# Kernel optimization log

Hardware: AMD Instinct MI355X
Metric: run time of the kernel (lower is better)

Reference implementation:

```python
import jax, jax.numpy as jnp
import numpy as np

N_E = 1024
E_DIM = 512
BETA = 0.25


def setup_inputs() -> dict:
    key = jax.random.key(0)
    k1, k2 = jax.random.split(key)
    z = jax.random.normal(k1, (16, E_DIM, 64, 64), dtype=jnp.float32)
    # nn.Embedding default init: N(0,1)
    codebook = jax.random.normal(k2, (N_E, E_DIM), dtype=jnp.float32)
    return {"z": z, "codebook": codebook}


def reference(z, codebook):
    # z: [B, C, H, W] -> [B, H, W, C]
    zp = jnp.transpose(z, (0, 2, 3, 1))
    B, H, W, C = zp.shape
    zf = zp.reshape(-1, C)  # [N, e_dim]
    d = (jnp.sum(zf * zf, axis=1, keepdims=True)
         + jnp.sum(codebook * codebook, axis=1)
         - 2.0 * zf @ codebook.T)
    idx = jnp.argmin(d, axis=1)  # [N]
    # one-hot @ codebook == gather
    z_q = codebook[idx].reshape(B, H, W, C)
    sg = jax.lax.stop_gradient
    e_latent_loss = jnp.mean((sg(z_q) - zp) ** 2)
    q_latent_loss = jnp.mean((z_q - sg(zp)) ** 2)
    codebook_loss = q_latent_loss + BETA * e_latent_loss
    # straight-through estimator
    z_q_st = zp + sg(z_q - zp)
    z_q_out = jnp.transpose(z_q_st, (0, 3, 1, 2))  # [B, C, H, W]
    indices = idx.reshape(B, 1, H, W)
    return (z_q_out, codebook_loss, indices)
```

## Files before the change

kernel.cpp:

```cpp
#include <hip/hip_runtime.h>

#define N_E    1024
#define E_DIM  512
#define BATCH  16
#define HW     4096
#define NROW   (BATCH * HW)
#define ZQ_SIZE (BATCH * E_DIM * HW)
#define LOSS_OFF ZQ_SIZE
#define IDX_OFF (ZQ_SIZE + 1)

typedef _Float16 half_t;
typedef __attribute__((ext_vector_type(2)))  __fp16   fp16x2;
typedef __attribute__((ext_vector_type(8)))  _Float16 frag8;
typedef __attribute__((ext_vector_type(16))) float    accv;

union U32H2 { fp16x2 h; uint32_t u; };
union FragU { uint32_t u[4]; frag8 f; };

static __device__ inline uint32_t pack2(float a, float b) {
    U32H2 t; t.h = __builtin_amdgcn_cvt_pkrtz(a, b); return t.u;
}

__global__ void k_prep(const float* __restrict__ cb,
                       float* __restrict__ cn,
                       float* __restrict__ ct,
                       unsigned long long* __restrict__ best) {
    __shared__ float t[32][33];
    int tx = threadIdx.x & 31;
    int ty = threadIdx.x >> 5;
    int jt = blockIdx.x & 31;
    int ctl = blockIdx.x >> 5;
    int j0 = jt * 32, c0 = ctl * 32;
    #pragma unroll
    for (int i = 0; i < 4; i++) {
        int row = ty + i * 8;
        t[row][tx] = cb[(size_t)(j0 + row) * E_DIM + c0 + tx];
    }
    __syncthreads();
    #pragma unroll
    for (int i = 0; i < 4; i++) {
        int row = ty + i * 8;
        ct[(size_t)(c0 + row) * N_E + j0 + tx] = t[tx][row];
    }

    if (blockIdx.x < 256) {
        int lane = threadIdx.x & 63;
        int wid  = threadIdx.x >> 6;
        int j = blockIdx.x * 4 + wid;
        const float* row = cb + (size_t)j * E_DIM;
        float s = 0.f;
        #pragma unroll
        for (int k = 0; k < E_DIM; k += 64) {
            float v = row[k + lane];
            s += v * v;
        }
        #pragma unroll
        for (int m = 32; m >= 1; m >>= 1) s += __shfl_xor(s, m);
        if (lane == 0) cn[j] = s;
    }

    int g = blockIdx.x * 256 + threadIdx.x;
    if (g < NROW) best[g] = 0xFFFFFFFFFFFFFFFFull;
}

#define ASTR 44
#define BSTR 40

__global__ __launch_bounds__(256, 2) void k_argmin_mfma(
        const float* __restrict__ z,
        const float* __restrict__ cb,
        const float* __restrict__ cn,
        unsigned long long* __restrict__ best) {
    __shared__ uint32_t aP[128 * ASTR];
    __shared__ half_t   bH[128 * BSTR];
    __shared__ half_t   bL[128 * BSTR];

    int tid  = threadIdx.x;
    int lane = tid & 63;
    int l31  = lane & 31;
    int lh   = lane >> 5;
    int wm   = (tid >> 6) & 1;
    int wg   = tid >> 7;

    int jt    = blockIdx.x & 7;
    int mtile = blockIdx.x >> 3;
    int n0  = mtile * 128;
    int b   = n0 >> 12;
    int hw0 = n0 & 4095;
    const float* zA = z + (size_t)b * E_DIM * HW + hw0 + 4 * (tid & 31);
    int a_kq = tid >> 5;
    int b_kq = tid & 7;
    int b_j0 = tid >> 3;

    accv acc[2][2];
    #pragma unroll
    for (int mt = 0; mt < 2; mt++)
        #pragma unroll
        for (int nt = 0; nt < 2; nt++)
            #pragma unroll
            for (int i = 0; i < 16; i++) acc[mt][nt][i] = 0.f;

    for (int ks = 0; ks < 16; ks++) {
        int c0 = ks * 32;
        __syncthreads();
        {
            uint32_t pk[4][4];
            #pragma unroll
            for (int i = 0; i < 4; i++) {
                int k = a_kq * 4 + i;
                float4 v = *(const float4*)(zA + (size_t)(c0 + k) * HW);
                uint32_t H01 = pack2(v.x, v.y);
                uint32_t H23 = pack2(v.z, v.w);
                U32H2 h01; h01.u = H01; U32H2 h23; h23.u = H23;
                uint32_t L01 = pack2(v.x - (float)h01.h.x, v.y - (float)h01.h.y);
                uint32_t L23 = pack2(v.z - (float)h23.h.x, v.w - (float)h23.h.y);
                pk[0][i] = __builtin_amdgcn_perm(L01, H01, 0x05040100u);
                pk[1][i] = __builtin_amdgcn_perm(L01, H01, 0x07060302u);
                pk[2][i] = __builtin_amdgcn_perm(L23, H23, 0x05040100u);
                pk[3][i] = __builtin_amdgcn_perm(L23, H23, 0x07060302u);
            }
            int m0 = (tid & 31) * 4;
            #pragma unroll
            for (int r = 0; r < 4; r++) {
                int row = m0 + r;
                int qs = a_kq ^ ((row >> 3) & 7);
                uint4 w = make_uint4(pk[r][0], pk[r][1], pk[r][2], pk[r][3]);
                *(uint4*)&aP[row * ASTR + qs * 4] = w;
            }
        }
        {
            const float* cbB = cb + (size_t)(jt * 128) * E_DIM + c0 + b_kq * 4;
            #pragma unroll
            for (int r = 0; r < 4; r++) {
                int jl = b_j0 + 32 * r;
                float4 v = *(const float4*)(cbB + (size_t)jl * E_DIM);
                uint32_t H01 = pack2(v.x, v.y);
                uint32_t H23 = pack2(v.z, v.w);
                U32H2 h01; h01.u = H01; U32H2 h23; h23.u = H23;
                uint32_t L01 = pack2(v.x - (float)h01.h.x, v.y - (float)h01.h.y);
                uint32_t L23 = pack2(v.z - (float)h23.h.x, v.w - (float)h23.h.y);
                *(uint2*)&bH[jl * BSTR + b_kq * 4] = make_uint2(H01, H23);
                *(uint2*)&bL[jl * BSTR + b_kq * 4] = make_uint2(L01, L23);
            }
        }
        __syncthreads();

        #pragma unroll
        for (int ks2 = 0; ks2 < 2; ks2++) {
            int k0 = ks2 * 16 + lh * 8;
            int q0 = k0 >> 2;
            frag8 ah[2], al[2];
            #pragma unroll
            for (int mt = 0; mt < 2; mt++) {
                int row = wm * 64 + mt * 32 + l31;
                int sw  = (row >> 3) & 7;
                const uint32_t* pr = &aP[row * ASTR];
                uint4 q0v = *(const uint4*)(pr + ((q0 ^ sw) << 2));
                uint4 q1v = *(const uint4*)(pr + (((q0 + 1) ^ sw) << 2));
                FragU uh, ul;
                uh.u[0] = __builtin_amdgcn_perm(q0v.y, q0v.x, 0x05040100u);
                uh.u[1] = __builtin_amdgcn_perm(q0v.w, q0v.z, 0x05040100u);
                uh.u[2] = __builtin_amdgcn_perm(q1v.y, q1v.x, 0x05040100u);
                uh.u[3] = __builtin_amdgcn_perm(q1v.w, q1v.z, 0x05040100u);
                ul.u[0] = __builtin_amdgcn_perm(q0v.y, q0v.x, 0x07060302u);
                ul.u[1] = __builtin_amdgcn_perm(q0v.w, q0v.z, 0x07060302u);
                ul.u[2] = __builtin_amdgcn_perm(q1v.y, q1v.x, 0x07060302u);
                ul.u[3] = __builtin_amdgcn_perm(q1v.w, q1v.z, 0x07060302u);
                ah[mt] = uh.f; al[mt] = ul.f;
            }
            frag8 bh[2], bl[2];
            #pragma unroll
            for (int nt = 0; nt < 2; nt++) {
                int n = wg * 64 + nt * 32 + l31;
                bh[nt] = *(const frag8*)&bH[n * BSTR + k0];
                bl[nt] = *(const frag8*)&bL[n * BSTR + k0];
            }
            #pragma unroll
            for (int mt = 0; mt < 2; mt++)
                #pragma unroll
                for (int nt = 0; nt < 2; nt++) {
                    acc[mt][nt] = __builtin_amdgcn_mfma_f32_32x32x16_f16(
                        ah[mt], bh[nt], acc[mt][nt], 0, 0, 0);
                    acc[mt][nt] = __builtin_amdgcn_mfma_f32_32x32x16_f16(
                        ah[mt], bl[nt], acc[mt][nt], 0, 0, 0);
                    acc[mt][nt] = __builtin_amdgcn_mfma_f32_32x32x16_f16(
                        al[mt], bh[nt], acc[mt][nt], 0, 0, 0);
                }
        }
    }

    int jbase = jt * 128 + wg * 64;
    float cn0 = cn[jbase + l31];
    float cn1 = cn[jbase + 32 + l31];
    int j0i = jbase + l31, j1i = jbase + 32 + l31;
    #pragma unroll
    for (int mt = 0; mt < 2; mt++) {
        #pragma unroll
        for (int r = 0; r < 16; r++) {
            float d0 = cn0 - 2.f * acc[mt][0][r];
            float d1 = cn1 - 2.f * acc[mt][1][r];
            float v; int ix;
            if (d1 < d0) { v = d1; ix = j1i; } else { v = d0; ix = j0i; }
            #pragma unroll
            for (int m = 1; m <= 16; m <<= 1) {
                float ov = __shfl_xor(v, m);
                int   oi = __shfl_xor(ix, m);
                if (ov < v || (ov == v && oi < ix)) { v = ov; ix = oi; }
            }
            if (l31 == r) {
                int row = wm * 64 + mt * 32 + (r & 3) + 8 * (r >> 2) + 4 * lh;
                uint32_t s = __float_as_uint(v);
                uint32_t k32 = (s & 0x80000000u) ? ~s : (s | 0x80000000u);
                unsigned long long key =
                    ((unsigned long long)k32 << 32) | (uint32_t)ix;
                atomicMin(&best[n0 + row], key);
            }
        }
    }
}

__global__ void k_gather_loss(const float* __restrict__ z,
                              const float* __restrict__ ct,
                              const unsigned long long* __restrict__ best,
                              float* __restrict__ out,
                              float* __restrict__ pl) {
    int g = blockIdx.x * blockDim.x + threadIdx.x;
    int w4 = g & 1023;
    int bc = g >> 10;
    int c  = bc & 511;
    int b  = bc >> 9;
    int n4 = b * 1024 + w4;

    ulonglong2 b01 = *(const ulonglong2*)(best + (size_t)n4 * 4);
    ulonglong2 b23 = *(const ulonglong2*)(best + (size_t)n4 * 4 + 2);
    int4 iv;
    iv.x = (int)(uint32_t)b01.x; iv.y = (int)(uint32_t)b01.y;
    iv.z = (int)(uint32_t)b23.x; iv.w = (int)(uint32_t)b23.y;

    const float* ctc = ct + (size_t)c * N_E;
    float4 zq;
    zq.x = ctc[iv.x]; zq.y = ctc[iv.y]; zq.z = ctc[iv.z]; zq.w = ctc[iv.w];
    float4 zv = *(const float4*)(z + (size_t)g * 4);

    float4 d;
    d.x = zq.x - zv.x; d.y = zq.y - zv.y; d.z = zq.z - zv.z; d.w = zq.w - zv.w;
    float4 o;
    o.x = zv.x + d.x; o.y = zv.y + d.y; o.z = zv.z + d.z; o.w = zv.w + d.w;
    *(float4*)(out + (size_t)g * 4) = o;

    float ls = d.x * d.x + d.y * d.y + d.z * d.z + d.w * d.w;
    #pragma unroll
    for (int m = 32; m >= 1; m >>= 1) ls += __shfl_xor(ls, m);

    __shared__ float wsum[4];
    int lane = threadIdx.x & 63, wid = threadIdx.x >> 6;
    if (lane == 0) wsum[wid] = ls;
    __syncthreads();
    if (threadIdx.x == 0)
        pl[blockIdx.x] = wsum[0] + wsum[1] + wsum[2] + wsum[3];

    if (c == 0) {
        float* ip = out + IDX_OFF + (size_t)n4 * 4;
        ip[0] = (float)iv.x; ip[1] = (float)iv.y;
        ip[2] = (float)iv.z; ip[3] = (float)iv.w;
    }
}

__global__ void k_final(const float* __restrict__ pl, float* __restrict__ out) {
    float s = 0.f;
    for (int i = threadIdx.x; i < 8192; i += 256) s += pl[i];
    #pragma unroll
    for (int m = 32; m >= 1; m >>= 1) s += __shfl_xor(s, m);
    __shared__ float wsum[4];
    int lane = threadIdx.x & 63, wid = threadIdx.x >> 6;
    if (lane == 0) wsum[wid] = s;
    __syncthreads();
    if (threadIdx.x == 0) {
        float tot = wsum[0] + wsum[1] + wsum[2] + wsum[3];
        out[LOSS_OFF] = 1.25f * tot / (float)ZQ_SIZE;
    }
}

extern "C" void kernel_launch(void* const* d_in, const int* in_sizes, int n_in,
                              void* d_out, int out_size, void* d_ws, size_t ws_size,
                              hipStream_t stream) {
    const float* z  = (const float*)d_in[0];
    const float* cb = (const float*)d_in[1];
    float* out = (float*)d_out;

    float* cn = (float*)d_ws + 16;
    float* ct = cn + 1024;
    unsigned long long* best =
        (unsigned long long*)(ct + 512 * 1024);
    float* pl = (float*)(best + NROW);

    k_prep<<<512, 256, 0, stream>>>(cb, cn, ct, best);
    k_argmin_mfma<<<4096, 256, 0, stream>>>(z, cb, cn, best);
    k_gather_loss<<<ZQ_SIZE / 4 / 256, 256, 0, stream>>>(z, ct, best, out, pl);
    k_final<<<1, 256, 0, stream>>>(pl, out);
}
```

Measured before the change: 560.4 us.

## Prepack codebook fp16 tiles and loop all codes per block with DMA pipeline

Precomputes the split fp16 high/low codebook tiles in a swizzled layout (stored temporarily in the output buffer) and makes each argmin block loop over all 1024 codes for its 128 rows. This removes the redundant per-block codebook conversion, the 64-bit atomicMin traffic and the best-key initialisation. Codebook tiles are double-buffered through direct global-to-LDS loads, with the z tile loaded into registers one stage ahead. The running minimum is kept in registers and resolved across waves in LDS. The trade-off is more register pressure and a grid of only 512 blocks, which may limit occupancy and latency hiding.

```diff
diff --git a/kernel.cpp b/kernel.cpp
--- a/kernel.cpp
+++ b/kernel.cpp
@@ -1,4 +1,5 @@
 #include <hip/hip_runtime.h>
+#include <stdint.h>
 
 #define N_E    1024
 #define E_DIM  512
@@ -15,65 +16,85 @@
 typedef __attribute__((ext_vector_type(16))) float    accv;
 
 union U32H2 { fp16x2 h; uint32_t u; };
-union FragU { uint32_t u[4]; frag8 f; };
 
 static __device__ inline uint32_t pack2(float a, float b) {
     U32H2 t; t.h = __builtin_amdgcn_cvt_pkrtz(a, b); return t.u;
 }
 
-__global__ void k_prep(const float* __restrict__ cb,
+static __device__ __forceinline__ void dma16(const void* g, void* l) {
+    __builtin_amdgcn_global_load_lds(
+        (const __attribute__((address_space(1))) void*)g,
+        (__attribute__((address_space(3))) void*)l,
+        16, 0, 0);
+}
+
+__global__ void k_pack(const float* __restrict__ cb,
+                       uint32_t* __restrict__ cbP,
                        float* __restrict__ cn,
-                       float* __restrict__ ct,
-                       unsigned long long* __restrict__ best) {
-    __shared__ float t[32][33];
-    int tx = threadIdx.x & 31;
-    int ty = threadIdx.x >> 5;
-    int jt = blockIdx.x & 31;
-    int ctl = blockIdx.x >> 5;
-    int j0 = jt * 32, c0 = ctl * 32;
-    #pragma unroll
-    for (int i = 0; i < 4; i++) {
-        int row = ty + i * 8;
-        t[row][tx] = cb[(size_t)(j0 + row) * E_DIM + c0 + tx];
-    }
-    __syncthreads();
-    #pragma unroll
-    for (int i = 0; i < 4; i++) {
-        int row = ty + i * 8;
-        ct[(size_t)(c0 + row) * N_E + j0 + tx] = t[tx][row];
-    }
-
-    if (blockIdx.x < 256) {
-        int lane = threadIdx.x & 63;
-        int wid  = threadIdx.x >> 6;
-        int j = blockIdx.x * 4 + wid;
-        const float* row = cb + (size_t)j * E_DIM;
-        float s = 0.f;
-        #pragma unroll
-        for (int k = 0; k < E_DIM; k += 64) {
-            float v = row[k + lane];
-            s += v * v;
-        }
-        #pragma unroll
-        for (int m = 32; m >= 1; m >>= 1) s += __shfl_xor(s, m);
-        if (lane == 0) cn[j] = s;
-    }
-
-    int g = blockIdx.x * 256 + threadIdx.x;
-    if (g < NROW) best[g] = 0xFFFFFFFFFFFFFFFFull;
-}
-
-#define ASTR 44
-#define BSTR 40
+                       float* __restrict__ ct) {
+    __shared__ float tsh[32][33];
+    int bidx = blockIdx.x;
+    int tid  = threadIdx.x;
+
+    if (bidx < 128) {
+        int jt = bidx >> 4, ks = bidx & 15;
+        int kq = tid & 7, jb = tid >> 3;
+        uint32_t* tile = cbP + (size_t)bidx * 4096;
+        int sH = kq >> 1, o = (kq & 1) * 2;
+        #pragma unroll
+        for (int r = 0; r < 4; r++) {
+            int j = jb + 32 * r;
+            float4 v = *(const float4*)(cb + (size_t)(jt * 128 + j) * E_DIM + ks * 32 + kq * 4);
+            uint32_t H01 = pack2(v.x, v.y);
+            uint32_t H23 = pack2(v.z, v.w);
+            U32H2 h01; h01.u = H01; U32H2 h23; h23.u = H23;
+            uint32_t L01 = pack2(v.x - (float)h01.h.x, v.y - (float)h01.h.y);
+            uint32_t L23 = pack2(v.z - (float)h23.h.x, v.w - (float)h23.h.y);
+            int dH = ((sH)     ^ (j & 7)) * 4 + o;
+            int dL = ((sH + 4) ^ (j & 7)) * 4 + o;
+            *(uint2*)(tile + j * 32 + dH) = make_uint2(H01, H23);
+            *(uint2*)(tile + j * 32 + dL) = make_uint2(L01, L23);
+        }
+    } else {
+        int pb = bidx - 128;
+        int tx = tid & 31, ty = tid >> 5;
+        int jtp = pb & 31, ctl = pb >> 5;
+        int j0 = jtp * 32, c0 = ctl * 32;
+        #pragma unroll
+        for (int i = 0; i < 4; i++) {
+            int row = ty + i * 8;
+            tsh[row][tx] = cb[(size_t)(j0 + row) * E_DIM + c0 + tx];
+        }
+        __syncthreads();
+        #pragma unroll
+        for (int i = 0; i < 4; i++) {
+            int row = ty + i * 8;
+            ct[(size_t)(c0 + row) * N_E + j0 + tx] = tsh[tx][row];
+        }
+        if (pb < 256) {
+            int lane = tid & 63;
+            int wvid = tid >> 6;
+            int j = pb * 4 + wvid;
+            const float* rowp = cb + (size_t)j * E_DIM;
+            float s = 0.f;
+            #pragma unroll
+            for (int k = 0; k < E_DIM; k += 64) {
+                float v = rowp[k + lane];
+                s += v * v;
+            }
+            #pragma unroll
+            for (int m = 32; m >= 1; m >>= 1) s += __shfl_xor(s, m);
+            if (lane == 0) cn[j] = s;
+        }
+    }
+}
 
 __global__ __launch_bounds__(256, 2) void k_argmin_mfma(
         const float* __restrict__ z,
-        const float* __restrict__ cb,
+        const uint32_t* __restrict__ cbP,
         const float* __restrict__ cn,
-        unsigned long long* __restrict__ best) {
-    __shared__ uint32_t aP[128 * ASTR];
-    __shared__ half_t   bH[128 * BSTR];
-    __shared__ half_t   bL[128 * BSTR];
+        uint32_t* __restrict__ bestIdx) {
+    __shared__ uint32_t lds[16384];
 
     int tid  = threadIdx.x;
     int lane = tid & 63;
@@ -81,16 +102,27 @@
     int lh   = lane >> 5;
     int wm   = (tid >> 6) & 1;
     int wg   = tid >> 7;
-
-    int jt    = blockIdx.x & 7;
-    int mtile = blockIdx.x >> 3;
-    int n0  = mtile * 128;
-    int b   = n0 >> 12;
-    int hw0 = n0 & 4095;
-    const float* zA = z + (size_t)b * E_DIM * HW + hw0 + 4 * (tid & 31);
-    int a_kq = tid >> 5;
-    int b_kq = tid & 7;
-    int b_j0 = tid >> 3;
+    int wid  = tid >> 6;
+
+    int n0  = blockIdx.x * 128;
+    int b   = n0 >> 12, hw0 = n0 & 4095;
+
+    int arow  = tid & 127;
+    int khalf = tid >> 7;
+    const float* zBase = z + (size_t)b * E_DIM * HW + hw0 + arow;
+
+    const char* cT  = (const char*)cbP;
+    int uoff  = wid * 4096;
+    int goffB = uoff + lane * 16;
+
+    float cnv[16];
+    #pragma unroll
+    for (int j = 0; j < 8; j++) {
+        cnv[2 * j]     = cn[j * 128 + wg * 64 + l31];
+        cnv[2 * j + 1] = cn[j * 128 + wg * 64 + 32 + l31];
+    }
+    #pragma unroll
+    for (int q = 0; q < 16; q++) asm volatile("" :: "v"(cnv[q]));
 
     accv acc[2][2];
     #pragma unroll
@@ -100,107 +132,147 @@
             #pragma unroll
             for (int i = 0; i < 16; i++) acc[mt][nt][i] = 0.f;
 
-    for (int ks = 0; ks < 16; ks++) {
-        int c0 = ks * 32;
-        __syncthreads();
+    float bv[2][16];
+    int   bi[2][16];
+    #pragma unroll
+    for (int mt = 0; mt < 2; mt++)
+        #pragma unroll
+        for (int r = 0; r < 16; r++) { bv[mt][r] = 1e30f; bi[mt][r] = 0; }
+
+    float rA[16];
+
+    #define ALOAD(q) do {                                                      \
+        int c0_ = ((q) & 15) * 32 + khalf * 16;                                \
+        _Pragma("unroll")                                                      \
+        for (int i = 0; i < 16; i++)                                           \
+            rA[i] = zBase[(size_t)(c0_ + i) * HW];                             \
+    } while (0)
+
+    #define ACONV(q) do {                                                      \
+        uint32_t* at_ = lds + ((q) & 1) * 8192;                                \
+        int sw_ = arow & 7;                                                    \
+        uint32_t h_[8], l_[8];                                                 \
+        _Pragma("unroll")                                                      \
+        for (int i2 = 0; i2 < 8; i2++) {                                       \
+            uint32_t H = pack2(rA[2 * i2], rA[2 * i2 + 1]);                    \
+            U32H2 hh; hh.u = H;                                                \
+            uint32_t L = pack2(rA[2 * i2]     - (float)hh.h.x,                 \
+                               rA[2 * i2 + 1] - (float)hh.h.y);                \
+            h_[i2] = H; l_[i2] = L;                                            \
+        }                                                                      \
+        int s0_ = khalf * 2;                                                   \
+        *(uint4*)&at_[arow * 32 + (((s0_    ) ^ sw_) << 2)] =                  \
+            make_uint4(h_[0], h_[1], h_[2], h_[3]);                            \
+        *(uint4*)&at_[arow * 32 + (((s0_ + 1) ^ sw_) << 2)] =                  \
+            make_uint4(h_[4], h_[5], h_[6], h_[7]);                            \
+        *(uint4*)&at_[arow * 32 + (((s0_ + 4) ^ sw_) << 2)] =                  \
+            make_uint4(l_[0], l_[1], l_[2], l_[3]);                            \
+        *(uint4*)&at_[arow * 32 + (((s0_ + 5) ^ sw_) << 2)] =                  \
+            make_uint4(l_[4], l_[5], l_[6], l_[7]);                            \
+    } while (0)
+
+    #define BSTAGE(q) do {                                                     \
+        char* lb_ = (char*)lds + ((q) & 1) * 32768 + 16384 + uoff;             \
+        const char* gb_ = cT + (size_t)(q) * 16384 + goffB;                    \
+        dma16(gb_,        lb_);                                                \
+        dma16(gb_ + 1024, lb_ + 1024);                                         \
+        dma16(gb_ + 2048, lb_ + 2048);                                         \
+        dma16(gb_ + 3072, lb_ + 3072);                                         \
+    } while (0)
+
+    ALOAD(0);
+    BSTAGE(0);
+    asm volatile("s_waitcnt vmcnt(4)" ::: "memory");
+    ACONV(0);
+    ALOAD(1);
+    asm volatile("s_waitcnt lgkmcnt(0)" ::: "memory");
+    asm volatile("s_waitcnt vmcnt(16)" ::: "memory");
+    __builtin_amdgcn_s_barrier();
+
+    #pragma unroll
+    for (int jt = 0; jt < 8; jt++) {
+        #pragma unroll 1
+        for (int ks = 0; ks < 16; ks++) {
+            int p = jt * 16 + ks, pn = p + 1;
+            if (pn < 128) {
+                BSTAGE(pn);
+                asm volatile("s_waitcnt vmcnt(4)" ::: "memory");
+                ACONV(pn);
+                if (pn < 127) ALOAD(pn + 1);
+            }
+
+            const uint32_t* A = lds + (p & 1) * 8192;
+            const uint32_t* B = A + 4096;
+            __builtin_amdgcn_s_setprio(1);
+            #pragma unroll
+            for (int ks2 = 0; ks2 < 2; ks2++) {
+                int s = ks2 * 2 + lh;
+                frag8 ah[2], al[2], bh[2], bl[2];
+                #pragma unroll
+                for (int mt = 0; mt < 2; mt++) {
+                    int row = wm * 64 + mt * 32 + l31;
+                    int sw = row & 7;
+                    ah[mt] = *(const frag8*)&A[row * 32 + ((s ^ sw) << 2)];
+                    al[mt] = *(const frag8*)&A[row * 32 + (((s + 4) ^ sw) << 2)];
+                }
+                #pragma unroll
+                for (int nt = 0; nt < 2; nt++) {
+                    int n = wg * 64 + nt * 32 + l31;
+                    int sw = n & 7;
+                    bh[nt] = *(const frag8*)&B[n * 32 + ((s ^ sw) << 2)];
+                    bl[nt] = *(const frag8*)&B[n * 32 + (((s + 4) ^ sw) << 2)];
+                }
+                #pragma unroll
+                for (int mt = 0; mt < 2; mt++)
+                    #pragma unroll
+                    for (int nt = 0; nt < 2; nt++)
+                        acc[mt][nt] = __builtin_amdgcn_mfma_f32_32x32x16_f16(
+                            ah[mt], bh[nt], acc[mt][nt], 0, 0, 0);
+                #pragma unroll
+                for (int mt = 0; mt < 2; mt++)
+                    #pragma unroll
+                    for (int nt = 0; nt < 2; nt++)
+                        acc[mt][nt] = __builtin_amdgcn_mfma_f32_32x32x16_f16(
+                            ah[mt], bl[nt], acc[mt][nt], 0, 0, 0);
+                #pragma unroll
+                for (int mt = 0; mt < 2; mt++)
+                    #pragma unroll
+                    for (int nt = 0; nt < 2; nt++)
+                        acc[mt][nt] = __builtin_amdgcn_mfma_f32_32x32x16_f16(
+                            al[mt], bh[nt], acc[mt][nt], 0, 0, 0);
+            }
+            __builtin_amdgcn_s_setprio(0);
+            asm volatile("s_waitcnt lgkmcnt(0)" ::: "memory");
+            if (pn < 128) {
+                if (pn < 127) asm volatile("s_waitcnt vmcnt(16)" ::: "memory");
+                else          asm volatile("s_waitcnt vmcnt(0)"  ::: "memory");
+                __builtin_amdgcn_s_barrier();
+            }
+        }
         {
-            uint32_t pk[4][4];
-            #pragma unroll
-            for (int i = 0; i < 4; i++) {
-                int k = a_kq * 4 + i;
-                float4 v = *(const float4*)(zA + (size_t)(c0 + k) * HW);
-                uint32_t H01 = pack2(v.x, v.y);
-                uint32_t H23 = pack2(v.z, v.w);
-                U32H2 h01; h01.u = H01; U32H2 h23; h23.u = H23;
-                uint32_t L01 = pack2(v.x - (float)h01.h.x, v.y - (float)h01.h.y);
-                uint32_t L23 = pack2(v.z - (float)h23.h.x, v.w - (float)h23.h.y);
-                pk[0][i] = __builtin_amdgcn_perm(L01, H01, 0x05040100u);
-                pk[1][i] = __builtin_amdgcn_perm(L01, H01, 0x07060302u);
-                pk[2][i] = __builtin_amdgcn_perm(L23, H23, 0x05040100u);
-                pk[3][i] = __builtin_amdgcn_perm(L23, H23, 0x07060302u);
-            }
-            int m0 = (tid & 31) * 4;
-            #pragma unroll
-            for (int r = 0; r < 4; r++) {
-                int row = m0 + r;
-                int qs = a_kq ^ ((row >> 3) & 7);
-                uint4 w = make_uint4(pk[r][0], pk[r][1], pk[r][2], pk[r][3]);
-                *(uint4*)&aP[row * ASTR + qs * 4] = w;
-            }
-        }
-        {
-            const float* cbB = cb + (size_t)(jt * 128) * E_DIM + c0 + b_kq * 4;
-            #pragma unroll
-            for (int r = 0; r < 4; r++) {
-                int jl = b_j0 + 32 * r;
-                float4 v = *(const float4*)(cbB + (size_t)jl * E_DIM);
-                uint32_t H01 = pack2(v.x, v.y);
-                uint32_t H23 = pack2(v.z, v.w);
-                U32H2 h01; h01.u = H01; U32H2 h23; h23.u = H23;
-                uint32_t L01 = pack2(v.x - (float)h01.h.x, v.y - (float)h01.h.y);
-                uint32_t L23 = pack2(v.z - (float)h23.h.x, v.w - (float)h23.h.y);
-                *(uint2*)&bH[jl * BSTR + b_kq * 4] = make_uint2(H01, H23);
-                *(uint2*)&bL[jl * BSTR + b_kq * 4] = make_uint2(L01, L23);
-            }
-        }
-        __syncthreads();
-
-        #pragma unroll
-        for (int ks2 = 0; ks2 < 2; ks2++) {
-            int k0 = ks2 * 16 + lh * 8;
-            int q0 = k0 >> 2;
-            frag8 ah[2], al[2];
-            #pragma unroll
-            for (int mt = 0; mt < 2; mt++) {
-                int row = wm * 64 + mt * 32 + l31;
-                int sw  = (row >> 3) & 7;
-                const uint32_t* pr = &aP[row * ASTR];
-                uint4 q0v = *(const uint4*)(pr + ((q0 ^ sw) << 2));
-                uint4 q1v = *(const uint4*)(pr + (((q0 + 1) ^ sw) << 2));
-                FragU uh, ul;
-                uh.u[0] = __builtin_amdgcn_perm(q0v.y, q0v.x, 0x05040100u);
-                uh.u[1] = __builtin_amdgcn_perm(q0v.w, q0v.z, 0x05040100u);
-                uh.u[2] = __builtin_amdgcn_perm(q1v.y, q1v.x, 0x05040100u);
-                uh.u[3] = __builtin_amdgcn_perm(q1v.w, q1v.z, 0x05040100u);
-                ul.u[0] = __builtin_amdgcn_perm(q0v.y, q0v.x, 0x07060302u);
-                ul.u[1] = __builtin_amdgcn_perm(q0v.w, q0v.z, 0x07060302u);
-                ul.u[2] = __builtin_amdgcn_perm(q1v.y, q1v.x, 0x07060302u);
-                ul.u[3] = __builtin_amdgcn_perm(q1v.w, q1v.z, 0x07060302u);
-                ah[mt] = uh.f; al[mt] = ul.f;
-            }
-            frag8 bh[2], bl[2];
-            #pragma unroll
-            for (int nt = 0; nt < 2; nt++) {
-                int n = wg * 64 + nt * 32 + l31;
-                bh[nt] = *(const frag8*)&bH[n * BSTR + k0];
-                bl[nt] = *(const frag8*)&bL[n * BSTR + k0];
-            }
+            float c0 = cnv[2 * jt], c1 = cnv[2 * jt + 1];
+            int j0i = jt * 128 + wg * 64 + l31;
+            int j1i = j0i + 32;
             #pragma unroll
             for (int mt = 0; mt < 2; mt++)
                 #pragma unroll
-                for (int nt = 0; nt < 2; nt++) {
-                    acc[mt][nt] = __builtin_amdgcn_mfma_f32_32x32x16_f16(
-                        ah[mt], bh[nt], acc[mt][nt], 0, 0, 0);
-                    acc[mt][nt] = __builtin_amdgcn_mfma_f32_32x32x16_f16(
-                        ah[mt], bl[nt], acc[mt][nt], 0, 0, 0);
-                    acc[mt][nt] = __builtin_amdgcn_mfma_f32_32x32x16_f16(
-                        al[mt], bh[nt], acc[mt][nt], 0, 0, 0);
+                for (int r = 0; r < 16; r++) {
+                    float d0 = c0 - 2.f * acc[mt][0][r];
+                    float d1 = c1 - 2.f * acc[mt][1][r];
+                    float v; int ix;
+                    if (d1 < d0) { v = d1; ix = j1i; } else { v = d0; ix = j0i; }
+                    if (v < bv[mt][r]) { bv[mt][r] = v; bi[mt][r] = ix; }
+                    acc[mt][0][r] = 0.f; acc[mt][1][r] = 0.f;
                 }
         }
     }
 
-    int jbase = jt * 128 + wg * 64;
-    float cn0 = cn[jbase + l31];
-    float cn1 = cn[jbase + 32 + l31];
-    int j0i = jbase + l31, j1i = jbase + 32 + l31;
-    #pragma unroll
-    for (int mt = 0; mt < 2; mt++) {
+    unsigned long long* red = (unsigned long long*)lds;
+    #pragma unroll
+    for (int mt = 0; mt < 2; mt++)
         #pragma unroll
         for (int r = 0; r < 16; r++) {
-            float d0 = cn0 - 2.f * acc[mt][0][r];
-            float d1 = cn1 - 2.f * acc[mt][1][r];
-            float v; int ix;
-            if (d1 < d0) { v = d1; ix = j1i; } else { v = d0; ix = j0i; }
+            float v = bv[mt][r]; int ix = bi[mt][r];
             #pragma unroll
             for (int m = 1; m <= 16; m <<= 1) {
                 float ov = __shfl_xor(v, m);
@@ -211,17 +283,24 @@
                 int row = wm * 64 + mt * 32 + (r & 3) + 8 * (r >> 2) + 4 * lh;
                 uint32_t s = __float_as_uint(v);
                 uint32_t k32 = (s & 0x80000000u) ? ~s : (s | 0x80000000u);
-                unsigned long long key =
+                red[wg * 128 + row] =
                     ((unsigned long long)k32 << 32) | (uint32_t)ix;
-                atomicMin(&best[n0 + row], key);
-            }
-        }
-    }
+            }
+        }
+    __syncthreads();
+    if (tid < 128) {
+        unsigned long long k0 = red[tid], k1 = red[128 + tid];
+        unsigned long long k = (k1 < k0) ? k1 : k0;
+        bestIdx[n0 + tid] = (uint32_t)k;
+    }
+    #undef ALOAD
+    #undef ACONV
+    #undef BSTAGE
 }
 
 __global__ void k_gather_loss(const float* __restrict__ z,
                               const float* __restrict__ ct,
-                              const unsigned long long* __restrict__ best,
+                              const uint32_t* __restrict__ bestIdx,
                               float* __restrict__ out,
                               float* __restrict__ pl) {
     int g = blockIdx.x * blockDim.x + threadIdx.x;
@@ -231,11 +310,7 @@
     int b  = bc >> 9;
     int n4 = b * 1024 + w4;
 
-    ulonglong2 b01 = *(const ulonglong2*)(best + (size_t)n4 * 4);
-    ulonglong2 b23 = *(const ulonglong2*)(best + (size_t)n4 * 4 + 2);
-    int4 iv;
-    iv.x = (int)(uint32_t)b01.x; iv.y = (int)(uint32_t)b01.y;
-    iv.z = (int)(uint32_t)b23.x; iv.w = (int)(uint32_t)b23.y;
+    uint4 iv = *(const uint4*)(bestIdx + (size_t)n4 * 4);
 
     const float* ctc = ct + (size_t)c * N_E;
     float4 zq;
@@ -253,8 +328,8 @@
     for (int m = 32; m >= 1; m >>= 1) ls += __shfl_xor(ls, m);
 
     __shared__ float wsum[4];
-    int lane = threadIdx.x & 63, wid = threadIdx.x >> 6;
-    if (lane == 0) wsum[wid] = ls;
+    int lane = threadIdx.x & 63, wvid = threadIdx.x >> 6;
+    if (lane == 0) wsum[wvid] = ls;
     __syncthreads();
     if (threadIdx.x == 0)
         pl[blockIdx.x] = wsum[0] + wsum[1] + wsum[2] + wsum[3];
@@ -272,8 +347,8 @@
     #pragma unroll
     for (int m = 32; m >= 1; m >>= 1) s += __shfl_xor(s, m);
     __shared__ float wsum[4];
-    int lane = threadIdx.x & 63, wid = threadIdx.x >> 6;
-    if (lane == 0) wsum[wid] = s;
+    int lane = threadIdx.x & 63, wvid = threadIdx.x >> 6;
+    if (lane == 0) wsum[wvid] = s;
     __syncthreads();
     if (threadIdx.x == 0) {
         float tot = wsum[0] + wsum[1] + wsum[2] + wsum[3];
@@ -284,18 +359,20 @@
 extern "C" void kernel_launch(void* const* d_in, const int* in_sizes, int n_in,
                               void* d_out, int out_size, void* d_ws, size_t ws_size,
                               hipStream_t stream) {
+    (void)in_sizes; (void)n_in; (void)out_size; (void)ws_size;
     const float* z  = (const float*)d_in[0];
     const float* cb = (const float*)d_in[1];
     float* out = (float*)d_out;
 
     float* cn = (float*)d_ws + 16;
     float* ct = cn + 1024;
-    unsigned long long* best =
-        (unsigned long long*)(ct + 512 * 1024);
-    float* pl = (float*)(best + NROW);
-
-    k_prep<<<512, 256, 0, stream>>>(cb, cn, ct, best);
-    k_argmin_mfma<<<4096, 256, 0, stream>>>(z, cb, cn, best);
-    k_gather_loss<<<ZQ_SIZE / 4 / 256, 256, 0, stream>>>(z, ct, best, out, pl);
+    uint32_t* bestIdx = (uint32_t*)(ct + 512 * 1024);
+    float* pl = (float*)(bestIdx + NROW);
+
+    uint32_t* cbP = (uint32_t*)d_out;
+
+    k_pack<<<640, 256, 0, stream>>>(cb, cbP, cn, ct);
+    k_argmin_mfma<<<512, 256, 0, stream>>>(z, cbP, cn, bestIdx);
+    k_gather_loss<<<ZQ_SIZE / 4 / 256, 256, 0, stream>>>(z, ct, bestIdx, out, pl);
     k_final<<<1, 256, 0, stream>>>(pl, out);
 }
```

Result: slower. 795.8 us (+42.0%).
